# Optimization experiments

Hardware: AMD Instinct MI355X
Metric: run time of the kernel (lower is better)

The kernel has to match this reference:

```python
import jax, jax.numpy as jnp
import numpy as np

EPS = 1e-07
BETA = 1.0
NEG_INF = -1e30


def setup_inputs() -> dict:
    key = jax.random.key(0)
    k1, k2 = jax.random.split(key)
    B, C = 262144, 128
    inputs = jax.random.normal(k1, (B, C), dtype=jnp.float32)
    targets = jax.random.randint(k2, (B,), 0, C, dtype=jnp.int64)
    return {"inputs": inputs, "targets": targets}


def reference(inputs, targets):
    B, C = inputs.shape
    dt = inputs.dtype
    probs = jax.nn.sigmoid(inputs)  # (B, C)

    # per-class counts (size_class in torch code)
    counts = jax.ops.segment_sum(jnp.ones((B,), dtype=dt), targets, num_segments=C)  # (C,)
    present = counts > 0
    safe_counts = jnp.where(present, counts, jnp.asarray(1.0, dt))

    # per-class mean of probs over samples with that label -> rows of mean_probs
    sum_probs = jax.ops.segment_sum(probs, targets, num_segments=C)  # (C, C)
    mean_probs = sum_probs / safe_counts[:, None]
    diag = jnp.arange(C)
    mean_probs = mean_probs.at[diag, diag].set(-1.0)  # mean_probs_k[k] = -1

    # positive term: mean over class-k samples of log(p[i,k]+eps), summed over present classes
    logp_pos_true = jnp.log(jnp.take_along_axis(probs, targets[:, None], axis=1)[:, 0] + EPS)  # (B,)
    pos_per_class = jax.ops.segment_sum(logp_pos_true, targets, num_segments=C) / safe_counts
    loss_pos = jnp.sum(jnp.where(present, pos_per_class, jnp.asarray(0.0, dt)))

    # per-class mean of log(1-p+eps) with the true-class column zeroed ((1-onehot) factor)
    logp_neg = jnp.log(1.0 - probs + EPS)  # (B, C)
    sum_logneg = jax.ops.segment_sum(logp_neg, targets, num_segments=C)  # (C, C)
    mean_loss_neg = (sum_logneg / safe_counts[:, None]).at[diag, diag].set(0.0)

    # negative term: per column k, softmax over present rows j != k of beta*mean_probs[j,k]
    mask = present[:, None] & (~jnp.eye(C, dtype=bool))  # rows j, cols k
    logits = jnp.where(mask, BETA * mean_probs, jnp.asarray(NEG_INF, dt))
    weights = jax.nn.softmax(logits, axis=0) * mask.astype(dt)  # zero weight when column fully masked
    loss_neg = jnp.sum(weights * mean_loss_neg)

    return -1.0 * (loss_pos + loss_neg)
```

## Files before the change

kernel.cpp:

```cpp
#include <hip/hip_runtime.h>
#include <math.h>

#define C      128
#define CAPLG  12
#define CAP    (1 << CAPLG)
#define SPLIT  16
#define NMB    (C * SPLIT)
#define SPB    1024
#define CSTR   16
#define LN2F   0.69314718056f

__device__ __forceinline__ float fast_rcp(float x) { return __builtin_amdgcn_rcpf(x); }

__global__ __launch_bounds__(256)
void scatter_kernel(const int* __restrict__ tgt, int* __restrict__ cursor2,
                    int* __restrict__ perm, int B) {
    __shared__ int lcur[C];
    __shared__ int sbase[C];
    if (threadIdx.x < C) lcur[threadIdx.x] = 0;
    __syncthreads();
    const int base = blockIdx.x * SPB;
    int myt[SPB / 256], myr[SPB / 256];
#pragma unroll
    for (int j = 0; j < SPB / 256; ++j) {
        int i = base + j * 256 + threadIdx.x;
        if (i < B) { myt[j] = tgt[i]; myr[j] = atomicAdd(&lcur[myt[j]], 1); }
        else myt[j] = -1;
    }
    __syncthreads();
    if (threadIdx.x < C)
        sbase[threadIdx.x] = atomicAdd(&cursor2[threadIdx.x * CSTR], lcur[threadIdx.x]);
    __syncthreads();
#pragma unroll
    for (int j = 0; j < SPB / 256; ++j)
        if (myt[j] >= 0)
            perm[(myt[j] << CAPLG) + sbase[myt[j]] + myr[j]] = base + j * 256 + threadIdx.x;
}

__global__ __launch_bounds__(256)
void main_kernel(const float* __restrict__ x, const int* __restrict__ perm,
                 const int* __restrict__ cursor2, float* __restrict__ partial) {
    const int k = blockIdx.x / SPLIT;
    const int p = blockIdx.x % SPLIT;
    const int n = min(cursor2[k * CSTR], CAP);
    const int chunk = (n + SPLIT - 1) / SPLIT;
    const int s0 = min(p * chunk, n);
    const int s1 = min(s0 + chunk, n);

    const int tid  = threadIdx.x;
    const int wave = tid >> 6;
    const int lane = tid & 63;
    const int half = lane >> 5;
    const int l5   = lane & 31;
    const int c0   = l5 << 2;
    const bool poslane = (l5 == (k >> 2));
    const int  ksub = k & 3;

    const int wlen = (s1 - s0 + 3) >> 2;
    const int ws0  = s0 + wave * wlen;
    const int ws1  = min(ws0 + wlen, s1);

    const int* bperm = perm + (k << CAPLG);

    float ap0=0,ap1=0,ap2=0,ap3=0;
    float sx0=0,sx1=0,sx2=0,sx3=0;
    float sl0=0,sl1=0,sl2=0,sl3=0;
    float apos = 0.f;

    for (int tbase = ws0; tbase < ws1; tbase += 64) {
        const int tl = min(64, ws1 - tbase);
        const int pv = (lane < tl) ? bperm[tbase + lane] : 0;
        const int h  = (tl + 1) >> 1;

        int iA = __shfl(pv, 0);
        int iB = __shfl(pv, (h < tl) ? h : 0);
        float4 cur = *reinterpret_cast<const float4*>(x + (size_t)(half ? iB : iA) * C + c0);
        float4 nxt = cur;
        if (h > 1) {
            iA = __shfl(pv, 1);
            iB = __shfl(pv, (1 + h < tl) ? 1 + h : 1);
            nxt = *reinterpret_cast<const float4*>(x + (size_t)(half ? iB : iA) * C + c0);
        }
        for (int j = 0; j < h; ++j) {
            float4 fut = cur;
            if (j + 2 < h) {
                iA = __shfl(pv, j + 2);
                iB = __shfl(pv, (j + 2 + h < tl) ? j + 2 + h : j + 2);
                fut = *reinterpret_cast<const float4*>(x + (size_t)(half ? iB : iA) * C + c0);
            }
            const bool valid = (half == 0) || (j + h < tl);
            if (valid) {
                float e, u, lu0, lu1, lu2, lu3;
                e = __expf(-cur.x); u = 1.f + e; lu0 = __log2f(u);
                ap0 += fast_rcp(u); sx0 += cur.x; sl0 += lu0;
                e = __expf(-cur.y); u = 1.f + e; lu1 = __log2f(u);
                ap1 += fast_rcp(u); sx1 += cur.y; sl1 += lu1;
                e = __expf(-cur.z); u = 1.f + e; lu2 = __log2f(u);
                ap2 += fast_rcp(u); sx2 += cur.z; sl2 += lu2;
                e = __expf(-cur.w); u = 1.f + e; lu3 = __log2f(u);
                ap3 += fast_rcp(u); sx3 += cur.w; sl3 += lu3;
                if (poslane) {
                    float lsel = (ksub & 2) ? ((ksub & 1) ? lu3 : lu2)
                                            : ((ksub & 1) ? lu1 : lu0);
                    apos += lsel;
                }
            }
            cur = nxt; nxt = fut;
        }
    }

    __shared__ __align__(16) float sP[8][C];
    __shared__ __align__(16) float sX[8][C];
    __shared__ __align__(16) float sL[8][C];
    __shared__ float sPos[8];
    const int g = (wave << 1) | half;
    *reinterpret_cast<float4*>(&sP[g][c0]) = make_float4(ap0, ap1, ap2, ap3);
    *reinterpret_cast<float4*>(&sX[g][c0]) = make_float4(sx0, sx1, sx2, sx3);
    *reinterpret_cast<float4*>(&sL[g][c0]) = make_float4(sl0, sl1, sl2, sl3);
    if (poslane) sPos[g] = apos;
    __syncthreads();

    const int bq = blockIdx.x;
    if (tid < C) {
        float s = 0.f;
#pragma unroll
        for (int g2 = 0; g2 < 8; ++g2) s += sP[g2][tid];
        partial[(size_t)tid * NMB + bq] = s;
    } else {
        const int t = tid - C;
        float sx = 0.f, sl = 0.f;
#pragma unroll
        for (int g2 = 0; g2 < 8; ++g2) { sx += sX[g2][t]; sl += sL[g2][t]; }
        partial[(size_t)(C + t) * NMB + bq] = -sx - LN2F * sl;
    }
    if (tid == 0) {
        float s = 0.f;
#pragma unroll
        for (int g2 = 0; g2 < 8; ++g2) s += sPos[g2];
        partial[(size_t)(2 * C) * NMB + bq] = -LN2F * s;
    }
}

__global__ __launch_bounds__(256)
void finalize_kernel(const float* __restrict__ partial, const int* __restrict__ cursor2,
                     float* __restrict__ colpart, int* __restrict__ ticket,
                     float* __restrict__ out) {
    const int k   = blockIdx.x;
    const int tid = threadIdx.x;

    __shared__ float spcol[C], slcol[C];
    __shared__ float sposr[16];

    {
        const int j    = tid >> 1;
        const int base = j * SPLIT + (tid & 1) * 8;
        const float4* rp = reinterpret_cast<const float4*>(partial + (size_t)k * NMB + base);
        const float4* rl = reinterpret_cast<const float4*>(partial + (size_t)(C + k) * NMB + base);
        float4 a = rp[0], b = rp[1];
        float accP = a.x + a.y + a.z + a.w + b.x + b.y + b.z + b.w;
        a = rl[0]; b = rl[1];
        float accL = a.x + a.y + a.z + a.w + b.x + b.y + b.z + b.w;
        accP += __shfl_xor(accP, 1);
        accL += __shfl_xor(accL, 1);
        if ((tid & 1) == 0) { spcol[j] = accP; slcol[j] = accL; }
        if (tid < SPLIT) sposr[tid] = partial[(size_t)(2 * C) * NMB + k * SPLIT + tid];
    }
    __syncthreads();

    if (tid < 64) {
        const int l = tid, j0 = l, j1 = l + 64;
        const float c0 = (float)cursor2[j0 * CSTR];
        const float c1 = (float)cursor2[j1 * CSTR];
        const bool  v0 = (j0 != k) && (c0 > 0.f);
        const bool  v1 = (j1 != k) && (c1 > 0.f);
        const float x0 = v0 ? spcol[j0] / c0 : -INFINITY;
        const float x1 = v1 ? spcol[j1] / c1 : -INFINITY;

        float m = fmaxf(x0, x1);
#pragma unroll
        for (int d = 1; d < 64; d <<= 1) m = fmaxf(m, __shfl_xor(m, d));

        float w0 = v0 ? __expf(x0 - m) : 0.f;
        float w1 = v1 ? __expf(x1 - m) : 0.f;
        float den = w0 + w1;
        float num = (v0 ? w0 * (slcol[j0] / c0) : 0.f)
                  + (v1 ? w1 * (slcol[j1] / c1) : 0.f);
#pragma unroll
        for (int d = 1; d < 64; d <<= 1) { den += __shfl_xor(den, d); num += __shfl_xor(num, d); }

        int last = 0;
        if (l == 0) {
            float colneg = (den > 0.f) ? num / den : 0.f;
            float ck     = (float)cursor2[k * CSTR];
            float ps     = 0.f;
#pragma unroll
            for (int q = 0; q < SPLIT; ++q) ps += sposr[q];
            float pk = (ck > 0.f) ? ps / ck : 0.f;
            colpart[k] = colneg + pk;
            __threadfence();
            last = (atomicAdd(ticket, 1) == C - 1);
        }
        last = __shfl(last, 0);
        if (last) {
            __threadfence();
            float s = colpart[l] + colpart[l + 64];
#pragma unroll
            for (int d = 1; d < 64; d <<= 1) s += __shfl_xor(s, d);
            if (l == 0) out[0] = -s;
        }
    }
}

extern "C" void kernel_launch(void* const* d_in, const int* in_sizes, int n_in,
                              void* d_out, int out_size, void* d_ws, size_t ws_size,
                              hipStream_t stream) {
    const float* x   = (const float*)d_in[0];
    const int*   tgt = (const int*)d_in[1];
    const int B = in_sizes[1];

    int*   cursor2 = (int*)d_ws;
    int*   ticket  = cursor2 + C * CSTR;
    int*   perm    = cursor2 + C * CSTR + CSTR;
    float* partial = (float*)(perm + C * CAP);
    float* colpart = partial + (size_t)(2 * C + 1) * NMB;

    hipMemsetAsync(cursor2, 0, (C * CSTR + CSTR) * sizeof(int), stream);
    scatter_kernel<<<(B + SPB - 1) / SPB, 256, 0, stream>>>(tgt, cursor2, perm, B);
    main_kernel<<<NMB, 256, 0, stream>>>(x, perm, cursor2, partial);
    finalize_kernel<<<C, 256, 0, stream>>>(partial, cursor2, colpart, ticket, (float*)d_out);
}
```

Measured before the change: 50.70 us.

## Use full-wave float2 row loads, block-major partials and vectorized target scatter

The main kernel now has each wave read a whole 128-float row per step, with each lane loading a float2 and a 3-deep prefetch, instead of splitting the wave into two half-waves that read float4 from different rows. The old 64-row chunk loop is dropped, so a wave loads its permutation indices once. Partial sums are written block-major (one contiguous 260-float record per block) and finalize is rewritten to gather them with strided reads at 128 threads. The scatter kernel reads targets as int4. This coarsens memory ops and simplifies indexing, but a wave now only handles rows that fit in one 64-lane index load, which assumes at most 64 rows per wave.

```diff
diff --git a/kernel.cpp b/kernel.cpp
--- a/kernel.cpp
+++ b/kernel.cpp
@@ -8,6 +8,7 @@
 #define NMB    (C * SPLIT)
 #define SPB    1024
 #define CSTR   16
+#define PBS    260
 #define LN2F   0.69314718056f
 
 __device__ __forceinline__ float fast_rcp(float x) { return __builtin_amdgcn_rcpf(x); }
@@ -19,129 +20,99 @@
     __shared__ int sbase[C];
     if (threadIdx.x < C) lcur[threadIdx.x] = 0;
     __syncthreads();
-    const int base = blockIdx.x * SPB;
-    int myt[SPB / 256], myr[SPB / 256];
-#pragma unroll
-    for (int j = 0; j < SPB / 256; ++j) {
-        int i = base + j * 256 + threadIdx.x;
-        if (i < B) { myt[j] = tgt[i]; myr[j] = atomicAdd(&lcur[myt[j]], 1); }
-        else myt[j] = -1;
-    }
+    const int base = blockIdx.x * SPB + threadIdx.x * 4;
+    int t0 = -1, t1 = -1, t2 = -1, t3 = -1;
+    if (base + 3 < B) {
+        int4 t4 = *reinterpret_cast<const int4*>(tgt + base);
+        t0 = t4.x; t1 = t4.y; t2 = t4.z; t3 = t4.w;
+    } else {
+        if (base     < B) t0 = tgt[base];
+        if (base + 1 < B) t1 = tgt[base + 1];
+        if (base + 2 < B) t2 = tgt[base + 2];
+        if (base + 3 < B) t3 = tgt[base + 3];
+    }
+    int r0 = (t0 >= 0) ? atomicAdd(&lcur[t0], 1) : 0;
+    int r1 = (t1 >= 0) ? atomicAdd(&lcur[t1], 1) : 0;
+    int r2 = (t2 >= 0) ? atomicAdd(&lcur[t2], 1) : 0;
+    int r3 = (t3 >= 0) ? atomicAdd(&lcur[t3], 1) : 0;
     __syncthreads();
     if (threadIdx.x < C)
         sbase[threadIdx.x] = atomicAdd(&cursor2[threadIdx.x * CSTR], lcur[threadIdx.x]);
     __syncthreads();
-#pragma unroll
-    for (int j = 0; j < SPB / 256; ++j)
-        if (myt[j] >= 0)
-            perm[(myt[j] << CAPLG) + sbase[myt[j]] + myr[j]] = base + j * 256 + threadIdx.x;
+    if (t0 >= 0) perm[(t0 << CAPLG) + sbase[t0] + r0] = base;
+    if (t1 >= 0) perm[(t1 << CAPLG) + sbase[t1] + r1] = base + 1;
+    if (t2 >= 0) perm[(t2 << CAPLG) + sbase[t2] + r2] = base + 2;
+    if (t3 >= 0) perm[(t3 << CAPLG) + sbase[t3] + r3] = base + 3;
 }
 
 __global__ __launch_bounds__(256)
 void main_kernel(const float* __restrict__ x, const int* __restrict__ perm,
                  const int* __restrict__ cursor2, float* __restrict__ partial) {
-    const int k = blockIdx.x / SPLIT;
-    const int p = blockIdx.x % SPLIT;
+    const int k = blockIdx.x >> 4;
+    const int p = blockIdx.x & (SPLIT - 1);
     const int n = min(cursor2[k * CSTR], CAP);
-    const int chunk = (n + SPLIT - 1) / SPLIT;
+    const int chunk = (n + SPLIT - 1) >> 4;
     const int s0 = min(p * chunk, n);
     const int s1 = min(s0 + chunk, n);
 
     const int tid  = threadIdx.x;
     const int wave = tid >> 6;
     const int lane = tid & 63;
-    const int half = lane >> 5;
-    const int l5   = lane & 31;
-    const int c0   = l5 << 2;
-    const bool poslane = (l5 == (k >> 2));
-    const int  ksub = k & 3;
+    const bool poslane = (lane == (k >> 1));
+    const int  kpar = k & 1;
 
     const int wlen = (s1 - s0 + 3) >> 2;
     const int ws0  = s0 + wave * wlen;
     const int ws1  = min(ws0 + wlen, s1);
+    const int wn   = (ws1 > ws0) ? (ws1 - ws0) : 0;
 
     const int* bperm = perm + (k << CAPLG);
-
-    float ap0=0,ap1=0,ap2=0,ap3=0;
-    float sx0=0,sx1=0,sx2=0,sx3=0;
-    float sl0=0,sl1=0,sl2=0,sl3=0;
+    const int pv = (lane < wn) ? bperm[ws0 + lane] : 0;
+
+    float ap0 = 0.f, ap1 = 0.f, sx0 = 0.f, sx1 = 0.f, sl0 = 0.f, sl1 = 0.f;
     float apos = 0.f;
 
-    for (int tbase = ws0; tbase < ws1; tbase += 64) {
-        const int tl = min(64, ws1 - tbase);
-        const int pv = (lane < tl) ? bperm[tbase + lane] : 0;
-        const int h  = (tl + 1) >> 1;
-
-        int iA = __shfl(pv, 0);
-        int iB = __shfl(pv, (h < tl) ? h : 0);
-        float4 cur = *reinterpret_cast<const float4*>(x + (size_t)(half ? iB : iA) * C + c0);
-        float4 nxt = cur;
-        if (h > 1) {
-            iA = __shfl(pv, 1);
-            iB = __shfl(pv, (1 + h < tl) ? 1 + h : 1);
-            nxt = *reinterpret_cast<const float4*>(x + (size_t)(half ? iB : iA) * C + c0);
-        }
-        for (int j = 0; j < h; ++j) {
-            float4 fut = cur;
-            if (j + 2 < h) {
-                iA = __shfl(pv, j + 2);
-                iB = __shfl(pv, (j + 2 + h < tl) ? j + 2 + h : j + 2);
-                fut = *reinterpret_cast<const float4*>(x + (size_t)(half ? iB : iA) * C + c0);
-            }
-            const bool valid = (half == 0) || (j + h < tl);
-            if (valid) {
-                float e, u, lu0, lu1, lu2, lu3;
-                e = __expf(-cur.x); u = 1.f + e; lu0 = __log2f(u);
-                ap0 += fast_rcp(u); sx0 += cur.x; sl0 += lu0;
-                e = __expf(-cur.y); u = 1.f + e; lu1 = __log2f(u);
-                ap1 += fast_rcp(u); sx1 += cur.y; sl1 += lu1;
-                e = __expf(-cur.z); u = 1.f + e; lu2 = __log2f(u);
-                ap2 += fast_rcp(u); sx2 += cur.z; sl2 += lu2;
-                e = __expf(-cur.w); u = 1.f + e; lu3 = __log2f(u);
-                ap3 += fast_rcp(u); sx3 += cur.w; sl3 += lu3;
-                if (poslane) {
-                    float lsel = (ksub & 2) ? ((ksub & 1) ? lu3 : lu2)
-                                            : ((ksub & 1) ? lu1 : lu0);
-                    apos += lsel;
-                }
-            }
-            cur = nxt; nxt = fut;
-        }
-    }
-
-    __shared__ __align__(16) float sP[8][C];
-    __shared__ __align__(16) float sX[8][C];
-    __shared__ __align__(16) float sL[8][C];
-    __shared__ float sPos[8];
-    const int g = (wave << 1) | half;
-    *reinterpret_cast<float4*>(&sP[g][c0]) = make_float4(ap0, ap1, ap2, ap3);
-    *reinterpret_cast<float4*>(&sX[g][c0]) = make_float4(sx0, sx1, sx2, sx3);
-    *reinterpret_cast<float4*>(&sL[g][c0]) = make_float4(sl0, sl1, sl2, sl3);
-    if (poslane) sPos[g] = apos;
-    __syncthreads();
-
-    const int bq = blockIdx.x;
+    if (wn > 0) {
+        const float* xl = x + 2 * lane;
+        float2 b0 = *reinterpret_cast<const float2*>(xl + (size_t)__shfl(pv, 0) * C);
+        float2 b1 = *reinterpret_cast<const float2*>(xl + (size_t)__shfl(pv, min(1, wn - 1)) * C);
+        float2 b2 = *reinterpret_cast<const float2*>(xl + (size_t)__shfl(pv, min(2, wn - 1)) * C);
+        for (int j = 0; j < wn; ++j) {
+            float2 cur = b0; b0 = b1; b1 = b2;
+            if (j + 3 < wn)
+                b2 = *reinterpret_cast<const float2*>(xl + (size_t)__shfl(pv, j + 3) * C);
+            float e0 = __expf(-cur.x), u0 = 1.f + e0, l0 = __log2f(u0);
+            float e1 = __expf(-cur.y), u1 = 1.f + e1, l1 = __log2f(u1);
+            ap0 += fast_rcp(u0); sx0 += cur.x; sl0 += l0;
+            ap1 += fast_rcp(u1); sx1 += cur.y; sl1 += l1;
+            if (poslane) apos += kpar ? l1 : l0;
+        }
+    }
+
+    __shared__ __align__(8) float sP[4][C];
+    __shared__ __align__(8) float sX[4][C];
+    __shared__ __align__(8) float sL[4][C];
+    __shared__ float sPos[4];
+    *reinterpret_cast<float2*>(&sP[wave][2 * lane]) = make_float2(ap0, ap1);
+    *reinterpret_cast<float2*>(&sX[wave][2 * lane]) = make_float2(sx0, sx1);
+    *reinterpret_cast<float2*>(&sL[wave][2 * lane]) = make_float2(sl0, sl1);
+    if (poslane) sPos[wave] = apos;
+    __syncthreads();
+
+    float* mine = partial + (size_t)blockIdx.x * PBS;
     if (tid < C) {
-        float s = 0.f;
-#pragma unroll
-        for (int g2 = 0; g2 < 8; ++g2) s += sP[g2][tid];
-        partial[(size_t)tid * NMB + bq] = s;
+        mine[tid] = sP[0][tid] + sP[1][tid] + sP[2][tid] + sP[3][tid];
     } else {
         const int t = tid - C;
-        float sx = 0.f, sl = 0.f;
-#pragma unroll
-        for (int g2 = 0; g2 < 8; ++g2) { sx += sX[g2][t]; sl += sL[g2][t]; }
-        partial[(size_t)(C + t) * NMB + bq] = -sx - LN2F * sl;
-    }
-    if (tid == 0) {
-        float s = 0.f;
-#pragma unroll
-        for (int g2 = 0; g2 < 8; ++g2) s += sPos[g2];
-        partial[(size_t)(2 * C) * NMB + bq] = -LN2F * s;
-    }
-}
-
-__global__ __launch_bounds__(256)
+        float sx = sX[0][t] + sX[1][t] + sX[2][t] + sX[3][t];
+        float sl = sL[0][t] + sL[1][t] + sL[2][t] + sL[3][t];
+        mine[C + t] = -sx - LN2F * sl;
+    }
+    if (tid == 0)
+        mine[256] = -LN2F * (sPos[0] + sPos[1] + sPos[2] + sPos[3]);
+}
+
+__global__ __launch_bounds__(128)
 void finalize_kernel(const float* __restrict__ partial, const int* __restrict__ cursor2,
                      float* __restrict__ colpart, int* __restrict__ ticket,
                      float* __restrict__ out) {
@@ -149,21 +120,20 @@
     const int tid = threadIdx.x;
 
     __shared__ float spcol[C], slcol[C];
-    __shared__ float sposr[16];
+    __shared__ float sposr[SPLIT];
 
     {
-        const int j    = tid >> 1;
-        const int base = j * SPLIT + (tid & 1) * 8;
-        const float4* rp = reinterpret_cast<const float4*>(partial + (size_t)k * NMB + base);
-        const float4* rl = reinterpret_cast<const float4*>(partial + (size_t)(C + k) * NMB + base);
-        float4 a = rp[0], b = rp[1];
-        float accP = a.x + a.y + a.z + a.w + b.x + b.y + b.z + b.w;
-        a = rl[0]; b = rl[1];
-        float accL = a.x + a.y + a.z + a.w + b.x + b.y + b.z + b.w;
-        accP += __shfl_xor(accP, 1);
-        accL += __shfl_xor(accL, 1);
-        if ((tid & 1) == 0) { spcol[j] = accP; slcol[j] = accL; }
-        if (tid < SPLIT) sposr[tid] = partial[(size_t)(2 * C) * NMB + k * SPLIT + tid];
+        const int j = tid;
+        const float* rowp = partial + (size_t)j * SPLIT * PBS;
+        float aP = 0.f, aL = 0.f;
+#pragma unroll
+        for (int q = 0; q < SPLIT; ++q) {
+            aP += rowp[q * PBS + k];
+            aL += rowp[q * PBS + C + k];
+        }
+        spcol[j] = aP; slcol[j] = aL;
+        if (tid < SPLIT)
+            sposr[tid] = partial[((size_t)k * SPLIT + tid) * PBS + 256];
     }
     __syncthreads();
 
@@ -222,10 +192,10 @@
     int*   ticket  = cursor2 + C * CSTR;
     int*   perm    = cursor2 + C * CSTR + CSTR;
     float* partial = (float*)(perm + C * CAP);
-    float* colpart = partial + (size_t)(2 * C + 1) * NMB;
+    float* colpart = partial + (size_t)NMB * PBS;
 
     hipMemsetAsync(cursor2, 0, (C * CSTR + CSTR) * sizeof(int), stream);
     scatter_kernel<<<(B + SPB - 1) / SPB, 256, 0, stream>>>(tgt, cursor2, perm, B);
     main_kernel<<<NMB, 256, 0, stream>>>(x, perm, cursor2, partial);
-    finalize_kernel<<<C, 256, 0, stream>>>(partial, cursor2, colpart, ticket, (float*)d_out);
-}
+    finalize_kernel<<<C, 128, 0, stream>>>(partial, cursor2, colpart, ticket, (float*)d_out);
+}
```

New measurement: 51.51 us. Within noise of the previous version (+1.6%).
